# Kernel optimization log

Measured on AMD Instinct MI355X. Metric: run time of the kernel, lower is better.

## Reference

```python
import jax, jax.numpy as jnp
import numpy as np

N_HEADS = 2

def setup_inputs() -> dict:
    key = jax.random.key(0)
    ks = jax.random.split(key, 10)
    d, bank, b, t = 192, 1000, 16, 4096
    s = 1.0 / np.sqrt(d)
    return {
        "z": jax.random.normal(ks[0], (b, d, t), jnp.float32),
        "memory_bank": jax.random.normal(ks[1], (d, bank), jnp.float32),
        "Wq": jax.random.normal(ks[2], (d, d), jnp.float32) * s,
        "bq": jax.random.normal(ks[3], (d,), jnp.float32) * 0.02,
        "Wk": jax.random.normal(ks[4], (d, d), jnp.float32) * s,
        "bk": jax.random.normal(ks[5], (d,), jnp.float32) * 0.02,
        "Wv": jax.random.normal(ks[6], (d, d), jnp.float32) * s,
        "bv": jax.random.normal(ks[7], (d,), jnp.float32) * 0.02,
        "Wo": jax.random.normal(ks[8], (d, d), jnp.float32) * s,
        "bo": jax.random.normal(ks[9], (d,), jnp.float32) * 0.02,
    }


def _split_heads(x):
    # x: [b, d, t] -> [b, h, t, dk]  (matches view(b, h, dk, t).transpose(2, 3))
    b, d, t = x.shape
    dk = d // N_HEADS
    return x.reshape(b, N_HEADS, dk, t).transpose(0, 1, 3, 2)


def reference(z, memory_bank, Wq, bq, Wk, bk, Wv, bv, Wo, bo):
    b, d, t = z.shape
    dk = d // N_HEADS
    # memory bank expanded over batch: [b, d, bank]
    c = jnp.broadcast_to(memory_bank[None], (b,) + memory_bank.shape)
    # 1x1 conv projections == per-channel linear
    q = jnp.einsum('oc,bct->bot', Wq, z) + bq[None, :, None]
    k = jnp.einsum('oc,bcs->bos', Wk, c) + bk[None, :, None]
    v = jnp.einsum('oc,bcs->bos', Wv, c) + bv[None, :, None]
    qh = _split_heads(q)  # [b, h, t, dk]
    kh = _split_heads(k)  # [b, h, bank, dk]
    vh = _split_heads(v)  # [b, h, bank, dk]
    scores = jnp.einsum('bhtd,bhsd->bhts', qh, kh) / jnp.sqrt(jnp.asarray(dk, z.dtype))
    p = jax.nn.softmax(scores, axis=-1)  # [b, h, t, bank]
    out = jnp.einsum('bhts,bhsd->bhtd', p, vh)  # [b, h, t, dk]
    out = out.transpose(0, 1, 3, 2).reshape(b, d, t)  # merge heads -> [b, d, t]
    return jnp.einsum('oc,bct->bot', Wo, out) + bo[None, :, None]
```

## Files before the change

kernel.cpp:

```cpp
#include <hip/hip_runtime.h>


typedef float  f32x4  __attribute__((ext_vector_type(4)));
typedef __bf16 bf16;
typedef __bf16 bf16x4 __attribute__((ext_vector_type(4)));
typedef __bf16 bf16x8 __attribute__((ext_vector_type(8)));

#define B_   16
#define D_   192
#define T_   4096
#define BANK 1000
#define SP   1024
#define DK   96
#define SCALE 0.10206207261596577f
#define LOG2E 1.4426950408889634f

__global__ __launch_bounds__(256) void kv_kernel(
    const float* __restrict__ mb, const float* __restrict__ Wk, const float* __restrict__ bk,
    const float* __restrict__ Wv, const float* __restrict__ bv,
    bf16* __restrict__ ktg, bf16* __restrict__ vtg) {
  int s = blockIdx.x * 256 + threadIdx.x;
  int o = blockIdx.y;
  int h = o / DK, i = o % DK;
  float ak = 0.f, av = 0.f;
  if (s < BANK) {
    ak = bk[o]; av = bv[o];
    for (int c = 0; c < D_; ++c) {
      float m = mb[c * BANK + s];
      ak += Wk[o * D_ + c] * m;
      av += Wv[o * D_ + c] * m;
    }
  }
  ktg[(size_t)(h * SP + s) * DK + i] = (bf16)ak;
  vtg[(size_t)(h * DK + i) * SP + s] = (bf16)av;
}

__global__ __launch_bounds__(256) void proj_kernel(
    const bf16* __restrict__ XT, const float* __restrict__ W,
    const float* __restrict__ bias, float* __restrict__ Y) {
  __shared__ __align__(16) char smem[24576];
  bf16* sB = (bf16*)smem;
  float* sE = (float*)smem;

  const int tid = threadIdx.x;
  const int t0 = blockIdx.x * 256, o0 = blockIdx.y * 64, b = blockIdx.z;
  const int lane = tid & 63, wv = tid >> 6;
  const int quad = lane >> 4, l15 = lane & 15;

  const bf16* ap[4];
#pragma unroll
  for (int m = 0; m < 4; ++m)
    ap[m] = &XT[((size_t)b * T_ + t0 + (wv * 4 + m) * 16 + l15) * D_ + quad * 8];
  bf16x8 acur[4];
#pragma unroll
  for (int m = 0; m < 4; ++m) acur[m] = *(const bf16x8*)ap[m];

#pragma unroll
  for (int r = 0; r < 6; ++r) {
    int g = tid + 256 * r;
    int kb = g >> 8, nt = (g >> 6) & 3, qd = (g >> 4) & 3, l5 = g & 15;
    const float* wp = &W[(o0 + nt * 16 + l5) * D_ + kb * 32 + qd * 8];
    f32x4 wa = *(const f32x4*)wp, wb = *(const f32x4*)(wp + 4);
    bf16x8 pk;
#pragma unroll
    for (int u = 0; u < 4; ++u) { pk[u] = (bf16)wa[u]; pk[4 + u] = (bf16)wb[u]; }
    *(bf16x8*)&sB[(size_t)g * 8] = pk;
  }

  f32x4 acc[4][4];
#pragma unroll
  for (int m = 0; m < 4; ++m)
#pragma unroll
    for (int n = 0; n < 4; ++n) acc[m][n] = (f32x4){0.f, 0.f, 0.f, 0.f};

  __syncthreads();
  for (int kb = 0; kb < 6; ++kb) {
    bf16x8 anext[4];
    if (kb < 5) {
#pragma unroll
      for (int m = 0; m < 4; ++m)
        anext[m] = *(const bf16x8*)(ap[m] + (kb + 1) * 32);
    }
    bf16x8 bf[4];
#pragma unroll
    for (int n = 0; n < 4; ++n)
      bf[n] = *(const bf16x8*)&sB[(size_t)((kb * 4 + n) * 64 + lane) * 8];
#pragma unroll
    for (int m = 0; m < 4; ++m)
#pragma unroll
      for (int n = 0; n < 4; ++n)
        acc[m][n] = __builtin_amdgcn_mfma_f32_16x16x32_bf16(acur[m], bf[n], acc[m][n], 0, 0, 0);
    if (kb < 5) {
#pragma unroll
      for (int m = 0; m < 4; ++m) acur[m] = anext[m];
    }
  }
  __syncthreads();

  float bs[4];
#pragma unroll
  for (int n = 0; n < 4; ++n) bs[n] = bias[o0 + n * 16 + l15];
  float* se = sE + wv * 1088;
#pragma unroll
  for (int m = 0; m < 4; ++m) {
#pragma unroll
    for (int n = 0; n < 4; ++n)
#pragma unroll
      for (int r = 0; r < 4; ++r)
        se[(quad * 4 + r) * 68 + n * 16 + l15] = acc[m][n][r] + bs[n];
#pragma unroll
    for (int p = 0; p < 4; ++p) {
      int o = p * 16 + (lane >> 2), tq = (lane & 3) * 4;
      f32x4 vv;
#pragma unroll
      for (int u = 0; u < 4; ++u) vv[u] = se[(tq + u) * 68 + o];
      *(f32x4*)&Y[((size_t)b * D_ + o0 + o) * T_ + t0 + wv * 64 + m * 16 + tq] = vv;
    }
  }
}

__global__ __launch_bounds__(256) void attn_kernel(
    const float* __restrict__ z, const float* __restrict__ Wq,
    const float* __restrict__ bq, const bf16* __restrict__ ktg,
    const bf16* __restrict__ vtg, bf16* __restrict__ owsT) {
  __shared__ __align__(16) char smem[40960];
  bf16* kt = (bf16*)smem;
  bf16* vt = (bf16*)(smem + 12288);
  bf16* sP = (bf16*)(smem + 24576);
  bf16* qt = (bf16*)smem;

  const int tid = threadIdx.x;
  const int t0 = blockIdx.x * 128, h = blockIdx.y, b = blockIdx.z;
  const int lane = tid & 63, wv = tid >> 6;
  const int quad = lane >> 4, l15 = lane & 15;

  const bf16* kb_g = ktg + (size_t)h * SP * DK;
  const bf16* vb_g = vtg + (size_t)h * DK * SP;
  const bf16* sp_ptr[6];
  int sp_str[6];
#pragma unroll
  for (int r = 0; r < 6; ++r) {
    int g = tid + 256 * r;
    if (g < 768) {
      int kb = g >> 8, n = (g >> 6) & 3, qd = (g >> 4) & 3, l5 = g & 15;
      sp_ptr[r] = kb_g + (size_t)(n * 16 + l5) * DK + kb * 32 + qd * 8;
      sp_str[r] = 64 * DK;
    } else {
      int gv = g - 768, blk = gv >> 6;
      int kbv = blk / 6, n = blk % 6, qd = (gv >> 4) & 3, l5 = gv & 15;
      sp_ptr[r] = vb_g + (size_t)(n * 16 + l5) * SP + kbv * 32 + qd * 8;
      sp_str[r] = 64;
    }
  }
  bf16x8 kreg[6];
#pragma unroll
  for (int r = 0; r < 6; ++r) kreg[r] = *(const bf16x8*)sp_ptr[r];

  f32x4 qacc[2][6];
#pragma unroll
  for (int t2 = 0; t2 < 2; ++t2)
#pragma unroll
    for (int n = 0; n < 6; ++n) qacc[t2][n] = (f32x4){0.f, 0.f, 0.f, 0.f};
  const float* zc0 = &z[((size_t)b * D_ + quad * 8) * T_ + t0 + wv * 32 + l15];
  const float* wrow = &Wq[(size_t)(h * DK + l15) * D_ + quad * 8];
  for (int kb = 0; kb < 6; ++kb) {
    bf16x8 zf[2];
#pragma unroll
    for (int t2 = 0; t2 < 2; ++t2)
#pragma unroll
      for (int j = 0; j < 8; ++j)
        zf[t2][j] = (bf16)zc0[(size_t)(kb * 32 + j) * T_ + t2 * 16];
#pragma unroll
    for (int n = 0; n < 6; ++n) {
      const float* wp = wrow + (size_t)n * 16 * D_ + kb * 32;
      f32x4 wa = *(const f32x4*)wp, wb = *(const f32x4*)(wp + 4);
      bf16x8 wf;
#pragma unroll
      for (int u = 0; u < 4; ++u) { wf[u] = (bf16)wa[u]; wf[4 + u] = (bf16)wb[u]; }
      qacc[0][n] = __builtin_amdgcn_mfma_f32_16x16x32_bf16(wf, zf[0], qacc[0][n], 0, 0, 0);
      qacc[1][n] = __builtin_amdgcn_mfma_f32_16x16x32_bf16(wf, zf[1], qacc[1][n], 0, 0, 0);
    }
  }
#pragma unroll
  for (int t2 = 0; t2 < 2; ++t2)
#pragma unroll
    for (int n = 0; n < 6; ++n) {
      f32x4 bq4 = *(const f32x4*)&bq[h * DK + n * 16 + quad * 4];
      int g = ((n & 1) * 2 + (quad >> 1)) * 16 + l15;
      int gs = g ^ ((g >> 3) & 7);
      bf16x4 pk;
#pragma unroll
      for (int r = 0; r < 4; ++r)
        pk[r] = (bf16)((qacc[t2][n][r] + bq4[r]) * (SCALE * LOG2E));
      *(bf16x4*)&qt[(size_t)(((n >> 1) * 8 + wv * 2 + t2) * 64 + gs) * 8 + (quad & 1) * 4] = pk;
    }
  bf16x8 qf[2][3];
#pragma unroll
  for (int t2 = 0; t2 < 2; ++t2)
#pragma unroll
    for (int kb = 0; kb < 3; ++kb)
      qf[t2][kb] = *(const bf16x8*)&qt[(size_t)((kb * 8 + wv * 2 + t2) * 64 +
                                                (lane ^ ((lane >> 3) & 7))) * 8];

  f32x4 oaccT[2][6];
#pragma unroll
  for (int t2 = 0; t2 < 2; ++t2)
#pragma unroll
    for (int n = 0; n < 6; ++n) oaccT[t2][n] = (f32x4){0.f, 0.f, 0.f, 0.f};
  float m_run[2] = {-1e30f, -1e30f}, l_run[2] = {0.f, 0.f};

  for (int ch = 0; ch < 16; ++ch) {
    __syncthreads();
#pragma unroll
    for (int r = 0; r < 6; ++r)
      *(bf16x8*)(smem + (size_t)(tid + 256 * r) * 16) = kreg[r];
    __syncthreads();
    if (ch < 15) {
#pragma unroll
      for (int r = 0; r < 6; ++r) {
        sp_ptr[r] += sp_str[r];
        kreg[r] = *(const bf16x8*)sp_ptr[r];
      }
    }

    f32x4 scT[2][4];
#pragma unroll
    for (int t2 = 0; t2 < 2; ++t2)
#pragma unroll
      for (int n = 0; n < 4; ++n) scT[t2][n] = (f32x4){0.f, 0.f, 0.f, 0.f};
#pragma unroll
    for (int kb = 0; kb < 3; ++kb) {
#pragma unroll
      for (int n = 0; n < 4; ++n) {
        bf16x8 kf = *(const bf16x8*)&kt[(size_t)((kb * 4 + n) * 64 + lane) * 8];
        scT[0][n] = __builtin_amdgcn_mfma_f32_16x16x32_bf16(kf, qf[0][kb], scT[0][n], 0, 0, 0);
        scT[1][n] = __builtin_amdgcn_mfma_f32_16x16x32_bf16(kf, qf[1][kb], scT[1][n], 0, 0, 0);
      }
    }
    if (ch == 15) {
#pragma unroll
      for (int t2 = 0; t2 < 2; ++t2)
#pragma unroll
        for (int r = 0; r < 4; ++r) {
          scT[t2][3][r] = -1e30f;
          if (quad >= 2) scT[t2][2][r] = -1e30f;
        }
    }

    float mt[2];
#pragma unroll
    for (int t2 = 0; t2 < 2; ++t2) {
      float m8[8];
#pragma unroll
      for (int u = 0; u < 8; ++u)
        m8[u] = fmaxf(scT[t2][u >> 1][(u & 1) * 2], scT[t2][u >> 1][(u & 1) * 2 + 1]);
      float ma = fmaxf(fmaxf(m8[0], m8[1]), fmaxf(m8[2], m8[3]));
      float mb2 = fmaxf(fmaxf(m8[4], m8[5]), fmaxf(m8[6], m8[7]));
      float m0 = fmaxf(ma, mb2);
      m0 = fmaxf(m0, __shfl_xor(m0, 16, 64));
      m0 = fmaxf(m0, __shfl_xor(m0, 32, 64));
      mt[t2] = m0;
    }
    if (!__all(mt[0] - m_run[0] <= 8.f && mt[1] - m_run[1] <= 8.f)) {
#pragma unroll
      for (int t2 = 0; t2 < 2; ++t2) {
        float mn = fmaxf(m_run[t2], mt[t2]);
        float al = exp2f(m_run[t2] - mn);
        m_run[t2] = mn;
        l_run[t2] *= al;
#pragma unroll
        for (int n = 0; n < 6; ++n)
#pragma unroll
          for (int r = 0; r < 4; ++r) oaccT[t2][n][r] *= al;
      }
    }
#pragma unroll
    for (int t2 = 0; t2 < 2; ++t2) {
      float pr[4][4];
#pragma unroll
      for (int n = 0; n < 4; ++n)
#pragma unroll
        for (int r = 0; r < 4; ++r) pr[n][r] = exp2f(scT[t2][n][r] - m_run[t2]);
      float s8[8];
#pragma unroll
      for (int u = 0; u < 8; ++u)
        s8[u] = pr[u >> 1][(u & 1) * 2] + pr[u >> 1][(u & 1) * 2 + 1];
      float ls = ((s8[0] + s8[1]) + (s8[2] + s8[3])) + ((s8[4] + s8[5]) + (s8[6] + s8[7]));
      ls += __shfl_xor(ls, 16, 64);
      ls += __shfl_xor(ls, 32, 64);
      l_run[t2] += ls;
#pragma unroll
      for (int kb2 = 0; kb2 < 2; ++kb2)
#pragma unroll
        for (int nh = 0; nh < 2; ++nh) {
          int n = kb2 * 2 + nh;
          int g = (nh * 2 + (quad >> 1)) * 16 + l15;
          int gs = g ^ ((g >> 3) & 7);
          bf16x4 pk = {(bf16)pr[n][0], (bf16)pr[n][1], (bf16)pr[n][2], (bf16)pr[n][3]};
          *(bf16x4*)&sP[(size_t)(((wv * 2 + t2) * 2 + kb2) * 64 + gs) * 8 +
                        (quad & 1) * 4] = pk;
        }
    }

#pragma unroll
    for (int kb2 = 0; kb2 < 2; ++kb2) {
      bf16x8 pa[2];
#pragma unroll
      for (int t2 = 0; t2 < 2; ++t2)
        pa[t2] = *(const bf16x8*)&sP[(size_t)(((wv * 2 + t2) * 2 + kb2) * 64 +
                                              (lane ^ ((lane >> 3) & 7))) * 8];
#pragma unroll
      for (int n2 = 0; n2 < 6; ++n2) {
        bf16x8 vf = *(const bf16x8*)&vt[(size_t)((kb2 * 6 + n2) * 64 + lane) * 8];
        oaccT[0][n2] = __builtin_amdgcn_mfma_f32_16x16x32_bf16(vf, pa[0], oaccT[0][n2], 0, 0, 0);
        oaccT[1][n2] = __builtin_amdgcn_mfma_f32_16x16x32_bf16(vf, pa[1], oaccT[1][n2], 0, 0, 0);
      }
    }
  }

#pragma unroll
  for (int t2 = 0; t2 < 2; ++t2) {
    float inv = 1.0f / l_run[t2];
    bf16* orow = &owsT[((size_t)b * T_ + t0 + wv * 32 + t2 * 16 + l15) * D_ +
                       h * DK + quad * 4];
#pragma unroll
    for (int n2 = 0; n2 < 6; ++n2) {
      bf16x4 pk = {(bf16)(oaccT[t2][n2][0] * inv), (bf16)(oaccT[t2][n2][1] * inv),
                   (bf16)(oaccT[t2][n2][2] * inv), (bf16)(oaccT[t2][n2][3] * inv)};
      *(bf16x4*)&orow[n2 * 16] = pk;
    }
  }
}

extern "C" void kernel_launch(void* const* d_in, const int* in_sizes, int n_in,
                              void* d_out, int out_size, void* d_ws, size_t ws_size,
                              hipStream_t stream) {
  const float* z  = (const float*)d_in[0];
  const float* mb = (const float*)d_in[1];
  const float* Wq = (const float*)d_in[2];
  const float* bq = (const float*)d_in[3];
  const float* Wk = (const float*)d_in[4];
  const float* bk = (const float*)d_in[5];
  const float* Wv = (const float*)d_in[6];
  const float* bv = (const float*)d_in[7];
  const float* Wo = (const float*)d_in[8];
  const float* bo = (const float*)d_in[9];
  float* out = (float*)d_out;

  bf16* ktg  = (bf16*)d_ws;
  bf16* vtg  = ktg + 2 * SP * DK;
  bf16* owsT = vtg + 2 * DK * SP;

  kv_kernel  <<<dim3(SP / 256, D_),    256, 0, stream>>>(mb, Wk, bk, Wv, bv, ktg, vtg);
  attn_kernel<<<dim3(T_ / 128, 2, B_), 256, 0, stream>>>(z, Wq, bq, ktg, vtg, owsT);
  proj_kernel<<<dim3(T_ / 256, 3, B_), 256, 0, stream>>>(owsT, Wo, bo, out);
}
```

Measured before the change: 245.2 us.

## Compute K/V projection with split-bf16 MFMA and raise attention occupancy hint

Rewrites the K/V projection kernel to use bf16 MFMA with a hi/lo split (three products) to approximate fp32 accuracy, with one wave per (K or V, head) pair and 16 bank columns per block. This replaces the scalar per-thread dot-product loop, which was launched over a 4x192 grid and re-read the memory bank for every output channel. The attention kernel also gains a launch_bounds min-blocks hint of 4, which may limit registers. The KV kernel is small relative to attention, so the overall gain is expected to be modest.

```diff
diff --git a/kernel.cpp b/kernel.cpp
--- a/kernel.cpp
+++ b/kernel.cpp
@@ -19,20 +19,65 @@
     const float* __restrict__ mb, const float* __restrict__ Wk, const float* __restrict__ bk,
     const float* __restrict__ Wv, const float* __restrict__ bv,
     bf16* __restrict__ ktg, bf16* __restrict__ vtg) {
-  int s = blockIdx.x * 256 + threadIdx.x;
-  int o = blockIdx.y;
-  int h = o / DK, i = o % DK;
-  float ak = 0.f, av = 0.f;
-  if (s < BANK) {
-    ak = bk[o]; av = bv[o];
-    for (int c = 0; c < D_; ++c) {
-      float m = mb[c * BANK + s];
-      ak += Wk[o * D_ + c] * m;
-      av += Wv[o * D_ + c] * m;
-    }
-  }
-  ktg[(size_t)(h * SP + s) * DK + i] = (bf16)ak;
-  vtg[(size_t)(h * DK + i) * SP + s] = (bf16)av;
+  const int tid = threadIdx.x;
+  const int lane = tid & 63, wv = tid >> 6;
+  const int quad = lane >> 4, l15 = lane & 15;
+  const int s0 = blockIdx.x * 16;
+  const int kvsel = wv >> 1, h = wv & 1;
+  const float* W  = kvsel ? Wv : Wk;
+  const float* bs = kvsel ? bv : bk;
+  const int s  = s0 + l15;
+  const int sc = s < BANK ? s : (BANK - 1);
+
+  f32x4 acc[6];
+#pragma unroll
+  for (int n = 0; n < 6; ++n) acc[n] = (f32x4){0.f, 0.f, 0.f, 0.f};
+
+  const float* wrow = &W[(size_t)(h * DK + l15) * D_ + quad * 8];
+  for (int kb = 0; kb < 6; ++kb) {
+    bf16x8 mhi, mlo;
+#pragma unroll
+    for (int j = 0; j < 8; ++j) {
+      float m = mb[(size_t)(kb * 32 + quad * 8 + j) * BANK + sc];
+      bf16 hi = (bf16)m;
+      mhi[j] = hi;
+      mlo[j] = (bf16)(m - (float)hi);
+    }
+#pragma unroll
+    for (int n = 0; n < 6; ++n) {
+      const float* wp = wrow + (size_t)n * 16 * D_ + kb * 32;
+      f32x4 wa = *(const f32x4*)wp, wb = *(const f32x4*)(wp + 4);
+      bf16x8 whi, wlo;
+#pragma unroll
+      for (int u = 0; u < 4; ++u) {
+        bf16 ha = (bf16)wa[u], hb = (bf16)wb[u];
+        whi[u] = ha;     wlo[u] = (bf16)(wa[u] - (float)ha);
+        whi[4 + u] = hb; wlo[4 + u] = (bf16)(wb[u] - (float)hb);
+      }
+      acc[n] = __builtin_amdgcn_mfma_f32_16x16x32_bf16(whi, mhi, acc[n], 0, 0, 0);
+      acc[n] = __builtin_amdgcn_mfma_f32_16x16x32_bf16(whi, mlo, acc[n], 0, 0, 0);
+      acc[n] = __builtin_amdgcn_mfma_f32_16x16x32_bf16(wlo, mhi, acc[n], 0, 0, 0);
+    }
+  }
+
+  if (kvsel == 0) {
+#pragma unroll
+    for (int n = 0; n < 6; ++n) {
+      f32x4 b4 = *(const f32x4*)&bs[h * DK + n * 16 + quad * 4];
+      bf16x4 pk;
+#pragma unroll
+      for (int r = 0; r < 4; ++r) pk[r] = (bf16)(acc[n][r] + b4[r]);
+      *(bf16x4*)&ktg[((size_t)(h * SP + s)) * DK + n * 16 + quad * 4] = pk;
+    }
+  } else {
+#pragma unroll
+    for (int n = 0; n < 6; ++n) {
+      f32x4 b4 = *(const f32x4*)&bs[h * DK + n * 16 + quad * 4];
+#pragma unroll
+      for (int r = 0; r < 4; ++r)
+        vtg[((size_t)(h * DK + n * 16 + quad * 4 + r)) * SP + s] = (bf16)(acc[n][r] + b4[r]);
+    }
+  }
 }
 
 __global__ __launch_bounds__(256) void proj_kernel(
@@ -119,7 +164,7 @@
   }
 }
 
-__global__ __launch_bounds__(256) void attn_kernel(
+__global__ __launch_bounds__(256, 4) void attn_kernel(
     const float* __restrict__ z, const float* __restrict__ Wq,
     const float* __restrict__ bq, const bf16* __restrict__ ktg,
     const bf16* __restrict__ vtg, bf16* __restrict__ owsT) {
@@ -351,7 +396,7 @@
   bf16* vtg  = ktg + 2 * SP * DK;
   bf16* owsT = vtg + 2 * DK * SP;
 
-  kv_kernel  <<<dim3(SP / 256, D_),    256, 0, stream>>>(mb, Wk, bk, Wv, bv, ktg, vtg);
+  kv_kernel  <<<dim3(SP / 16),         256, 0, stream>>>(mb, Wk, bk, Wv, bv, ktg, vtg);
   attn_kernel<<<dim3(T_ / 128, 2, B_), 256, 0, stream>>>(z, Wq, bq, ktg, vtg, owsT);
   proj_kernel<<<dim3(T_ / 256, 3, B_), 256, 0, stream>>>(owsT, Wo, bo, out);
 }
```

After: 431.5 us. 76.0% more time.
